# Kernel optimization log

Measured on AMD Instinct MI355X. Metric: run time of the kernel, lower is better.

## Reference

```python
import jax, jax.numpy as jnp
import numpy as np

N_NODES = 20000
N_EDGES = 150000
D_IN = 512
D_OUT = 512
BN_EPS = 1e-5


def setup_inputs() -> dict:
    key = jax.random.key(0)
    k1, k2, k3, k4 = jax.random.split(key, 4)
    x = jax.random.normal(k1, (N_NODES, D_IN), dtype=jnp.float32)
    src = jax.random.randint(k2, (N_EDGES,), 0, N_NODES, dtype=jnp.int64)
    dst = jax.random.randint(k3, (N_EDGES,), 0, N_NODES, dtype=jnp.int64)
    # Linear params (PyTorch layout: W is [out, in], y = x @ W.T + b)
    W = jax.random.normal(k4, (D_OUT, D_IN), dtype=jnp.float32) * (1.0 / np.sqrt(D_IN))
    b = jnp.zeros((D_OUT,), dtype=jnp.float32)
    gamma = jnp.ones((D_OUT,), dtype=jnp.float32)
    beta = jnp.zeros((D_OUT,), dtype=jnp.float32)
    return {"x": x, "src": src, "dst": dst, "W": W, "b": b, "gamma": gamma, "beta": beta}


def reference(x, src, dst, W, b, gamma, beta):
    n = x.shape[0]
    # send_and_recv over all edges: copy src feature, sum-reduce at dst.
    agg = jax.ops.segment_sum(x[src], dst, num_segments=n)  # [N, D_IN]
    indeg = jax.ops.segment_sum(jnp.ones(dst.shape, dtype=x.dtype), dst, num_segments=n)
    # Nodes with no incoming edges keep their original feature (DGL semantics).
    h = jnp.where(indeg[:, None] > 0, agg, x)
    # Linear + activation
    h = jnp.einsum('nd,od->no', h, W) + b
    h = jax.nn.relu(h)
    # BatchNorm1d (training mode: batch statistics, biased variance)
    mean = jnp.mean(h, axis=0)
    var = jnp.var(h, axis=0)
    h = (h - mean) * jax.lax.rsqrt(var + BN_EPS) * gamma + beta
    # Dropout is stochastic; reference uses eval-mode identity.
    return h
```

## Files before the change

kernel.cpp:

```cpp
#include <hip/hip_runtime.h>
#include <hip/hip_bf16.h>

#define N_NODES 20000
#define N_EDGES 150000
#define D 512
#define MPAD 20096
#define BN_EPS 1e-5f

typedef __attribute__((ext_vector_type(8))) short s16x8;
typedef __attribute__((ext_vector_type(4))) float f32x4;

__device__ __forceinline__ short f2bf(float f) {
    union { float f; unsigned u; } v; v.f = f;
    unsigned r = (v.u + 0x7fff + ((v.u >> 16) & 1)) >> 16;
    return (short)r;
}
__device__ __forceinline__ float bf2f(short b) {
    union { unsigned u; float f; } c;
    c.u = ((unsigned)(unsigned short)b) << 16;
    return c.f;
}
__device__ __forceinline__ s16x8 cvt8(const float* p) {
    float4 a = *(const float4*)p;
    float4 b = *(const float4*)(p + 4);
    s16x8 o;
    o[0] = f2bf(a.x); o[1] = f2bf(a.y); o[2] = f2bf(a.z); o[3] = f2bf(a.w);
    o[4] = f2bf(b.x); o[5] = f2bf(b.y); o[6] = f2bf(b.z); o[7] = f2bf(b.w);
    return o;
}

__device__ __forceinline__ void load_lds16(const short* g, short* l) {
    __builtin_amdgcn_global_load_lds((const __attribute__((address_space(1))) void*)g,
                                     (__attribute__((address_space(3))) void*)l, 16, 0, 0);
}

#define WCH (D * D / 8)
#define XCH (N_NODES * D / 8)
#define CONVCH (WCH + XCH)
#define ZCH 5120
__global__ __launch_bounds__(256) void convert_wx_zero(const float* __restrict__ W,
                                                       const float* __restrict__ x,
                                                       short* __restrict__ Wb,
                                                       short* __restrict__ Xb,
                                                       int* __restrict__ count) {
    int c = blockIdx.x * 256 + threadIdx.x;
    if (c < WCH) {
        *(s16x8*)(Wb + (size_t)c * 8) = cvt8(W + (size_t)c * 8);
    } else if (c < CONVCH) {
        size_t idx = (size_t)(c - WCH) * 8;
        *(s16x8*)(Xb + idx) = cvt8(x + idx);
    } else {
        int z = c - CONVCH;
        if (z * 4 < N_NODES) *(int4*)(count + z * 4) = make_int4(0, 0, 0, 0);
    }
}

__global__ __launch_bounds__(256) void count_edges(const int* __restrict__ dst,
                                                   int* __restrict__ count) {
    int i = blockIdx.x * 256 + threadIdx.x;
    if (i * 8 < N_EDGES) {
        int4 a = *(const int4*)(dst + i * 8);
        int4 b = *(const int4*)(dst + i * 8 + 4);
        atomicAdd(&count[a.x], 1); atomicAdd(&count[a.y], 1);
        atomicAdd(&count[a.z], 1); atomicAdd(&count[a.w], 1);
        atomicAdd(&count[b.x], 1); atomicAdd(&count[b.y], 1);
        atomicAdd(&count[b.z], 1); atomicAdd(&count[b.w], 1);
    }
}

__global__ __launch_bounds__(1024) void scan_csr(const int* __restrict__ count,
                                                 int* __restrict__ rowstart,
                                                 int* __restrict__ cursor,
                                                 float* __restrict__ colsum,
                                                 float* __restrict__ colsumsq) {
    __shared__ int partial[1024];
    int t = threadIdx.x;
    if (t < D) colsum[t] = 0.f;
    else if (t < 2 * D) colsumsq[t - D] = 0.f;

    int v[20];
    int s = 0;
    if (t < 1000) {
        const int4* p = (const int4*)(count + t * 20);
        #pragma unroll
        for (int j = 0; j < 5; ++j) {
            int4 q = p[j];
            v[j * 4 + 0] = q.x; v[j * 4 + 1] = q.y;
            v[j * 4 + 2] = q.z; v[j * 4 + 3] = q.w;
        }
        #pragma unroll
        for (int j = 0; j < 20; ++j) s += v[j];
    }
    partial[t] = s;
    __syncthreads();
    for (int off = 1; off < 1024; off <<= 1) {
        int p2 = (t >= off) ? partial[t - off] : 0;
        __syncthreads();
        partial[t] += p2;
        __syncthreads();
    }
    if (t < 1000) {
        int run = (t == 0) ? 0 : partial[t - 1];
        int rs[20];
        #pragma unroll
        for (int j = 0; j < 20; ++j) { rs[j] = run; run += v[j]; }
        int4* rp = (int4*)(rowstart + t * 20);
        int4* cp = (int4*)(cursor + t * 20);
        #pragma unroll
        for (int j = 0; j < 5; ++j) {
            int4 q = make_int4(rs[j * 4], rs[j * 4 + 1], rs[j * 4 + 2], rs[j * 4 + 3]);
            rp[j] = q;
            cp[j] = q;
        }
    }
    if (t == 1023) rowstart[N_NODES] = partial[1023];
}

__global__ __launch_bounds__(256) void fill_edges(const int* __restrict__ src,
                                                  const int* __restrict__ dst,
                                                  int* __restrict__ cursor,
                                                  int* __restrict__ esrc) {
    int i = blockIdx.x * 256 + threadIdx.x;
    if (i < N_EDGES) {
        int p = atomicAdd(&cursor[dst[i]], 1);
        esrc[p] = src[i];
    }
}

__global__ __launch_bounds__(256) void gather_bf16(const short* __restrict__ Xb,
                                                   const int* __restrict__ rowstart,
                                                   const int* __restrict__ esrc,
                                                   short* __restrict__ Ab) {
    int node = (blockIdx.x * 256 + threadIdx.x) >> 6;
    int lane = threadIdx.x & 63;
    if (node >= MPAD) return;
    size_t cb = (size_t)lane * 8;
    s16x8 o;
    if (node >= N_NODES) {
        o = (s16x8)0;
    } else {
        int e0 = rowstart[node], e1 = rowstart[node + 1];
        if (e0 == e1) {
            o = *(const s16x8*)(Xb + (size_t)node * D + cb);
        } else {
            float a0[8] = {}, a1[8] = {}, a2[8] = {}, a3[8] = {};
            int e = e0;
            for (; e + 3 < e1; e += 4) {
                int s0 = esrc[e], s1 = esrc[e + 1], s2 = esrc[e + 2], s3 = esrc[e + 3];
                s16x8 v0 = *(const s16x8*)(Xb + (size_t)s0 * D + cb);
                s16x8 v1 = *(const s16x8*)(Xb + (size_t)s1 * D + cb);
                s16x8 v2 = *(const s16x8*)(Xb + (size_t)s2 * D + cb);
                s16x8 v3 = *(const s16x8*)(Xb + (size_t)s3 * D + cb);
                #pragma unroll
                for (int i = 0; i < 8; ++i) a0[i] += bf2f(v0[i]);
                #pragma unroll
                for (int i = 0; i < 8; ++i) a1[i] += bf2f(v1[i]);
                #pragma unroll
                for (int i = 0; i < 8; ++i) a2[i] += bf2f(v2[i]);
                #pragma unroll
                for (int i = 0; i < 8; ++i) a3[i] += bf2f(v3[i]);
            }
            if (e < e1) {
                s16x8 v0 = *(const s16x8*)(Xb + (size_t)esrc[e] * D + cb);
                #pragma unroll
                for (int i = 0; i < 8; ++i) a0[i] += bf2f(v0[i]);
            }
            if (e + 1 < e1) {
                s16x8 v1 = *(const s16x8*)(Xb + (size_t)esrc[e + 1] * D + cb);
                #pragma unroll
                for (int i = 0; i < 8; ++i) a1[i] += bf2f(v1[i]);
            }
            if (e + 2 < e1) {
                s16x8 v2 = *(const s16x8*)(Xb + (size_t)esrc[e + 2] * D + cb);
                #pragma unroll
                for (int i = 0; i < 8; ++i) a2[i] += bf2f(v2[i]);
            }
            #pragma unroll
            for (int i = 0; i < 8; ++i) o[i] = f2bf((a0[i] + a1[i]) + (a2[i] + a3[i]));
        }
    }
    *(s16x8*)(Ab + (size_t)node * D + cb) = o;
}

#define BM 128
#define BNT 128
#define BK 32

__global__ __launch_bounds__(256) void gemm_relu_stats(const short* __restrict__ A,
                                                       const short* __restrict__ B,
                                                       const float* __restrict__ bias,
                                                       short* __restrict__ h,
                                                       float* __restrict__ colsum,
                                                       float* __restrict__ colsumsq) {
    __shared__ short As[BM * BK];
    __shared__ short Bs[BNT * BK];
    int tid = threadIdx.x;
    int lane = tid & 63;
    int wave = tid >> 6;
    int wr = wave >> 1, wc = wave & 1;
    int m0 = blockIdx.x * BM;
    int n0 = blockIdx.y * BNT;

    f32x4 acc[4][4] = {};

    int srow = lane >> 2;
    int scol = (lane & 3) * 8;
    const short* Ag = A + (size_t)(m0 + wave * 32 + srow) * D + scol;
    const short* Bg = B + (size_t)(n0 + wave * 32 + srow) * D + scol;
    short* Asl = As + wave * 1024;
    short* Bsl = Bs + wave * 1024;

    for (int kt = 0; kt < D; kt += BK) {
        #pragma unroll
        for (int j = 0; j < 2; ++j) {
            load_lds16(Ag + (size_t)j * 16 * D + kt, Asl + j * 512);
            load_lds16(Bg + (size_t)j * 16 * D + kt, Bsl + j * 512);
        }
        __syncthreads();
        s16x8 af[4], bfr[4];
        int ko = (lane >> 4) * 8;
        #pragma unroll
        for (int m = 0; m < 4; ++m)
            af[m] = *(const s16x8*)(As + (wr * 64 + m * 16 + (lane & 15)) * BK + ko);
        #pragma unroll
        for (int n = 0; n < 4; ++n)
            bfr[n] = *(const s16x8*)(Bs + (wc * 64 + n * 16 + (lane & 15)) * BK + ko);
        #pragma unroll
        for (int m = 0; m < 4; ++m)
            #pragma unroll
            for (int n = 0; n < 4; ++n)
                acc[m][n] = __builtin_amdgcn_mfma_f32_16x16x32_bf16(af[m], bfr[n], acc[m][n], 0, 0, 0);
        __syncthreads();
    }

    #pragma unroll
    for (int n = 0; n < 4; ++n) {
        int col = n0 + wc * 64 + n * 16 + (lane & 15);
        float bv = bias[col];
        float s = 0.f, q = 0.f;
        #pragma unroll
        for (int m = 0; m < 4; ++m) {
            int rbase = m0 + wr * 64 + m * 16 + (lane >> 4) * 4;
            #pragma unroll
            for (int r = 0; r < 4; ++r) {
                int row = rbase + r;
                if (row < N_NODES) {
                    float v = acc[m][n][r] + bv;
                    v = v > 0.f ? v : 0.f;
                    h[(size_t)row * D + col] = f2bf(v);
                    s += v;
                    q += v * v;
                }
            }
        }
        s += __shfl_xor(s, 16, 64);
        s += __shfl_xor(s, 32, 64);
        q += __shfl_xor(q, 16, 64);
        q += __shfl_xor(q, 32, 64);
        if (lane < 16) {
            atomicAdd(&colsum[col], s);
            atomicAdd(&colsumsq[col], q);
        }
    }
}

__global__ __launch_bounds__(256) void bn_apply(const short* __restrict__ h,
                                                float* __restrict__ out,
                                                const float* __restrict__ colsum,
                                                const float* __restrict__ colsumsq,
                                                const float* __restrict__ gamma,
                                                const float* __restrict__ beta) {
    __shared__ float s_scale[D], s_shift[D];
    for (int c = threadIdx.x; c < D; c += 256) {
        float mean = colsum[c] * (1.f / N_NODES);
        float var = colsumsq[c] * (1.f / N_NODES) - mean * mean;
        float rs = rsqrtf(var + BN_EPS);
        float sc = gamma[c] * rs;
        s_scale[c] = sc;
        s_shift[c] = beta[c] - mean * sc;
    }
    __syncthreads();
    const int total = N_NODES * D / 8;
    for (int i = blockIdx.x * 256 + threadIdx.x; i < total; i += gridDim.x * 256) {
        s16x8 hv = ((const s16x8*)h)[i];
        int c0 = (i * 8) & (D - 1);
        float4 o0, o1;
        o0.x = bf2f(hv[0]) * s_scale[c0]     + s_shift[c0];
        o0.y = bf2f(hv[1]) * s_scale[c0 + 1] + s_shift[c0 + 1];
        o0.z = bf2f(hv[2]) * s_scale[c0 + 2] + s_shift[c0 + 2];
        o0.w = bf2f(hv[3]) * s_scale[c0 + 3] + s_shift[c0 + 3];
        o1.x = bf2f(hv[4]) * s_scale[c0 + 4] + s_shift[c0 + 4];
        o1.y = bf2f(hv[5]) * s_scale[c0 + 5] + s_shift[c0 + 5];
        o1.z = bf2f(hv[6]) * s_scale[c0 + 6] + s_shift[c0 + 6];
        o1.w = bf2f(hv[7]) * s_scale[c0 + 7] + s_shift[c0 + 7];
        ((float4*)out)[i * 2]     = o0;
        ((float4*)out)[i * 2 + 1] = o1;
    }
}

extern "C" void kernel_launch(void* const* d_in, const int* in_sizes, int n_in,
                              void* d_out, int out_size, void* d_ws, size_t ws_size,
                              hipStream_t stream) {
    const float* x     = (const float*)d_in[0];
    const int*   src   = (const int*)d_in[1];
    const int*   dst   = (const int*)d_in[2];
    const float* W     = (const float*)d_in[3];
    const float* bias  = (const float*)d_in[4];
    const float* gamma = (const float*)d_in[5];
    const float* beta  = (const float*)d_in[6];
    float* out = (float*)d_out;

    char* ws = (char*)d_ws;
    size_t off = 0;
    float* colsum   = (float*)(ws + off); off += D * 4;
    float* colsumsq = (float*)(ws + off); off += D * 4;
    int*   rowstart = (int*)(ws + off);   off += (size_t)(N_NODES + 4) * 4;
    int*   cursor   = (int*)(ws + off);   off += (size_t)N_NODES * 4;
    int*   count    = (int*)(ws + off);   off += (size_t)ZCH * 16;
    int*   esrc     = (int*)(ws + off);   off += (size_t)N_EDGES * 4;
    off = (off + 255) & ~(size_t)255;
    short* Wb       = (short*)(ws + off); off += (size_t)D * D * 2;
    short* Xb       = (short*)(ws + off); off += (size_t)N_NODES * D * 2;
    short* Ab       = (short*)(ws + off); off += (size_t)MPAD * D * 2;
    short* hbuf     = (short*)(ws + off); off += (size_t)N_NODES * D * 2;

    convert_wx_zero<<<dim3((CONVCH + ZCH) / 256), dim3(256), 0, stream>>>(W, x, Wb, Xb, count);
    count_edges<<<dim3((N_EDGES / 8 + 255) / 256), dim3(256), 0, stream>>>(dst, count);
    scan_csr<<<dim3(1), dim3(1024), 0, stream>>>(count, rowstart, cursor, colsum, colsumsq);
    fill_edges<<<dim3((N_EDGES + 255) / 256), dim3(256), 0, stream>>>(src, dst, cursor, esrc);
    gather_bf16<<<dim3(MPAD / 4), dim3(256), 0, stream>>>(Xb, rowstart, esrc, Ab);
    gemm_relu_stats<<<dim3(MPAD / BM, D / BNT), dim3(256), 0, stream>>>(Ab, Wb, bias, hbuf, colsum, colsumsq);
    bn_apply<<<dim3(2048), dim3(256), 0, stream>>>(hbuf, out, colsum, colsumsq, gamma, beta);
}
```

Before: 111.4 us.

## Fuse GEMM and BatchNorm apply via cooperative grid sync

Replaces the separate GEMM+ReLU+stats kernel and BN-apply kernel with one cooperative kernel. Each block keeps its accumulator tile in registers, adds column statistics atomically, waits on a grid-wide barrier, then applies the normalization and writes fp32 output directly. This removes the bf16 intermediate round-trip and one launch. It needs the whole 157x4 grid to be co-resident, otherwise it falls back to the old two-kernel path. Register pressure and the cost of the grid barrier are the risks.

Result: slower. 180.1 us (+61.7%).

```diff
diff --git a/kernel.cpp b/kernel.cpp
--- a/kernel.cpp
+++ b/kernel.cpp
@@ -1,5 +1,8 @@
 #include <hip/hip_runtime.h>
 #include <hip/hip_bf16.h>
+#include <hip/hip_cooperative_groups.h>
+
+namespace cg = cooperative_groups;
 
 #define N_NODES 20000
 #define N_EDGES 150000
@@ -186,6 +189,114 @@
 #define BNT 128
 #define BK 32
 
+__global__ __launch_bounds__(256) void gemm_bn_fused(const short* __restrict__ A,
+                                                     const short* __restrict__ B,
+                                                     const float* __restrict__ bias,
+                                                     float* __restrict__ out,
+                                                     float* __restrict__ colsum,
+                                                     float* __restrict__ colsumsq,
+                                                     const float* __restrict__ gamma,
+                                                     const float* __restrict__ beta) {
+    __shared__ short As[BM * BK];
+    __shared__ short Bs[BNT * BK];
+    __shared__ float s_scale[BNT], s_shift[BNT];
+    int tid = threadIdx.x;
+    int lane = tid & 63;
+    int wave = tid >> 6;
+    int wr = wave >> 1, wc = wave & 1;
+    int m0 = blockIdx.x * BM;
+    int n0 = blockIdx.y * BNT;
+
+    f32x4 acc[4][4] = {};
+
+    int srow = lane >> 2;
+    int scol = (lane & 3) * 8;
+    const short* Ag = A + (size_t)(m0 + wave * 32 + srow) * D + scol;
+    const short* Bg = B + (size_t)(n0 + wave * 32 + srow) * D + scol;
+    short* Asl = As + wave * 1024;
+    short* Bsl = Bs + wave * 1024;
+
+    for (int kt = 0; kt < D; kt += BK) {
+        #pragma unroll
+        for (int j = 0; j < 2; ++j) {
+            load_lds16(Ag + (size_t)j * 16 * D + kt, Asl + j * 512);
+            load_lds16(Bg + (size_t)j * 16 * D + kt, Bsl + j * 512);
+        }
+        __syncthreads();
+        s16x8 af[4], bfr[4];
+        int ko = (lane >> 4) * 8;
+        #pragma unroll
+        for (int m = 0; m < 4; ++m)
+            af[m] = *(const s16x8*)(As + (wr * 64 + m * 16 + (lane & 15)) * BK + ko);
+        #pragma unroll
+        for (int n = 0; n < 4; ++n)
+            bfr[n] = *(const s16x8*)(Bs + (wc * 64 + n * 16 + (lane & 15)) * BK + ko);
+        #pragma unroll
+        for (int m = 0; m < 4; ++m)
+            #pragma unroll
+            for (int n = 0; n < 4; ++n)
+                acc[m][n] = __builtin_amdgcn_mfma_f32_16x16x32_bf16(af[m], bfr[n], acc[m][n], 0, 0, 0);
+        __syncthreads();
+    }
+
+    #pragma unroll
+    for (int n = 0; n < 4; ++n) {
+        int col = n0 + wc * 64 + n * 16 + (lane & 15);
+        float bv = bias[col];
+        float s = 0.f, q = 0.f;
+        #pragma unroll
+        for (int m = 0; m < 4; ++m) {
+            int rbase = m0 + wr * 64 + m * 16 + (lane >> 4) * 4;
+            #pragma unroll
+            for (int r = 0; r < 4; ++r) {
+                float v = acc[m][n][r] + bv;
+                v = v > 0.f ? v : 0.f;
+                acc[m][n][r] = v;
+                if (rbase + r < N_NODES) { s += v; q += v * v; }
+            }
+        }
+        s += __shfl_xor(s, 16, 64);
+        s += __shfl_xor(s, 32, 64);
+        q += __shfl_xor(q, 16, 64);
+        q += __shfl_xor(q, 32, 64);
+        if (lane < 16) {
+            atomicAdd(&colsum[col], s);
+            atomicAdd(&colsumsq[col], q);
+        }
+    }
+
+    cg::this_grid().sync();
+
+    if (tid < BNT) {
+        int c = n0 + tid;
+        float cs = __hip_atomic_load(&colsum[c], __ATOMIC_RELAXED, __HIP_MEMORY_SCOPE_AGENT);
+        float cq = __hip_atomic_load(&colsumsq[c], __ATOMIC_RELAXED, __HIP_MEMORY_SCOPE_AGENT);
+        float mean = cs * (1.f / N_NODES);
+        float var = cq * (1.f / N_NODES) - mean * mean;
+        float rs = rsqrtf(var + BN_EPS);
+        float sc = gamma[c] * rs;
+        s_scale[tid] = sc;
+        s_shift[tid] = beta[c] - mean * sc;
+    }
+    __syncthreads();
+
+    #pragma unroll
+    for (int n = 0; n < 4; ++n) {
+        int lcol = wc * 64 + n * 16 + (lane & 15);
+        float sc = s_scale[lcol], sh = s_shift[lcol];
+        int col = n0 + lcol;
+        #pragma unroll
+        for (int m = 0; m < 4; ++m) {
+            int rbase = m0 + wr * 64 + m * 16 + (lane >> 4) * 4;
+            #pragma unroll
+            for (int r = 0; r < 4; ++r) {
+                int row = rbase + r;
+                if (row < N_NODES) out[(size_t)row * D + col] = acc[m][n][r] * sc + sh;
+            }
+        }
+    }
+}
+
 __global__ __launch_bounds__(256) void gemm_relu_stats(const short* __restrict__ A,
                                                        const short* __restrict__ B,
                                                        const float* __restrict__ bias,
@@ -329,6 +440,21 @@
     scan_csr<<<dim3(1), dim3(1024), 0, stream>>>(count, rowstart, cursor, colsum, colsumsq);
     fill_edges<<<dim3((N_EDGES + 255) / 256), dim3(256), 0, stream>>>(src, dst, cursor, esrc);
     gather_bf16<<<dim3(MPAD / 4), dim3(256), 0, stream>>>(Xb, rowstart, esrc, Ab);
-    gemm_relu_stats<<<dim3(MPAD / BM, D / BNT), dim3(256), 0, stream>>>(Ab, Wb, bias, hbuf, colsum, colsumsq);
-    bn_apply<<<dim3(2048), dim3(256), 0, stream>>>(hbuf, out, colsum, colsumsq, gamma, beta);
-}
+
+    const short* Ab_c = Ab;
+    const short* Wb_c = Wb;
+    const float* bias_c = bias;
+    float* out_c = out;
+    float* colsum_c = colsum;
+    float* colsumsq_c = colsumsq;
+    const float* gamma_c = gamma;
+    const float* beta_c = beta;
+    void* args[8] = { &Ab_c, &Wb_c, &bias_c, &out_c, &colsum_c, &colsumsq_c, &gamma_c, &beta_c };
+    hipError_t err = hipLaunchCooperativeKernel((const void*)gemm_bn_fused,
+                                                dim3(MPAD / BM, D / BNT), dim3(256),
+                                                args, 0, stream);
+    if (err != hipSuccess) {
+        gemm_relu_stats<<<dim3(MPAD / BM, D / BNT), dim3(256), 0, stream>>>(Ab, Wb, bias, hbuf, colsum, colsumsq);
+        bn_apply<<<dim3(2048), dim3(256), 0, stream>>>(hbuf, out, colsum, colsumsq, gamma, beta);
+    }
+}
```
